# Kernel optimization log

Hardware: AMD Instinct MI355X
Metric: run time of the kernel (lower is better)

Reference implementation:

```python
import jax, jax.numpy as jnp
import numpy as np

LINK_LEN = 3
LN_EPS = 1e-5


def _layer_norm(x, w, b):
    mu = jnp.mean(x, axis=-1, keepdims=True)
    var = jnp.var(x, axis=-1, keepdims=True)
    return (x - mu) * jax.lax.rsqrt(var + LN_EPS) * w + b


def setup_inputs() -> dict:
    key = jax.random.key(0)
    ks = jax.random.split(key, 7)
    B, LAG, N, DIN, E, H = 16, 12, 5000, 32, 64, 64
    HH = H // 2
    return {
        "x": jax.random.normal(ks[0], (B, N, DIN), jnp.float32),
        "x_window": jax.random.normal(ks[1], (B, LAG, N, DIN // 2), jnp.float32),
        "node_embeddings": jax.random.normal(ks[2], (N, E), jnp.float32),
        "weights_pool": jax.random.normal(ks[3], (E, LINK_LEN, DIN, HH), jnp.float32) * 0.1,
        "weights_window": jax.random.normal(ks[4], (E, DIN // 2, HH), jnp.float32) * 0.1,
        "bias_pool": jax.random.normal(ks[5], (E, H), jnp.float32) * 0.1,
        "T": jax.random.normal(ks[6], (LAG,), jnp.float32),
        "ln1_w": jnp.ones((HH,), jnp.float32),
        "ln1_b": jnp.zeros((HH,), jnp.float32),
        "ln2_w": jnp.ones((HH,), jnp.float32),
        "ln2_b": jnp.zeros((HH,), jnp.float32),
    }


def reference(x, x_window, node_embeddings, weights_pool, weights_window,
              bias_pool, T, ln1_w, ln1_b, ln2_w, ln2_b):
    N = node_embeddings.shape[0]
    # adaptive adjacency: softmax(relu(E E^T)) over rows' neighbors (dim=1)
    supports = jax.nn.softmax(jax.nn.relu(node_embeddings @ node_embeddings.T), axis=1)
    support_set = [jnp.eye(N, dtype=x.dtype), supports]
    for k in range(2, LINK_LEN):
        support_set.append(supports @ support_set[k - 1])
    S = jnp.stack(support_set, axis=0)                      # [k, N, N]
    # per-node dynamic weights / bias from embeddings
    weights = jnp.einsum('nd,dkio->nkio', node_embeddings, weights_pool)  # [N,k,DIN,HH]
    bias = node_embeddings @ bias_pool                                     # [N,H]
    # graph conv path
    x_g = jnp.einsum('knm,bmc->bnkc', S, x)                 # [B,N,k,DIN]
    x_gconv = jnp.einsum('bnki,nkio->bno', x_g, weights)    # [B,N,HH]
    # temporal window path
    ww = jnp.einsum('nd,dio->nio', node_embeddings, weights_window)        # [N,DIN/2,HH]
    x_w = jnp.einsum('btni,nio->bnot', x_window, ww)        # [B,N,HH,LAG]
    x_wconv = x_w @ T                                       # [B,N,HH]
    out = jnp.concatenate([_layer_norm(x_gconv, ln1_w, ln1_b),
                           _layer_norm(x_wconv, ln2_w, ln2_b)], axis=-1) + bias
    return out
```

## Files before the change

kernel.cpp:

```cpp
#include <hip/hip_runtime.h>
#include <hip/hip_bf16.h>

#define NN   5000
#define EDIM 64
#define DINC 32
#define BB   16
#define LAGN 12
#define BC   512
#define KPAD 5120

typedef __attribute__((ext_vector_type(8))) short short8;
typedef __attribute__((ext_vector_type(4))) float float4v;

static __device__ __forceinline__ ushort f2bf(float x) {
  __hip_bfloat16 h = __float2bfloat16(x);
  return *reinterpret_cast<ushort*>(&h);
}
static __device__ __forceinline__ float bf2f(ushort u) {
  unsigned int x = ((unsigned int)u) << 16;
  return __uint_as_float(x);
}
static __device__ __forceinline__ short8 cvt8(const float* p) {
  const float4 v0 = *(const float4*)p, v1 = *(const float4*)(p + 4);
  short8 r;
  r[0] = (short)f2bf(v0.x); r[1] = (short)f2bf(v0.y);
  r[2] = (short)f2bf(v0.z); r[3] = (short)f2bf(v0.w);
  r[4] = (short)f2bf(v1.x); r[5] = (short)f2bf(v1.y);
  r[6] = (short)f2bf(v1.z); r[7] = (short)f2bf(v1.w);
  return r;
}

static __device__ __forceinline__ void gll16(const ushort* g, ushort* l) {
  __builtin_amdgcn_global_load_lds(
      (const __attribute__((address_space(1))) void*)g,
      (__attribute__((address_space(3))) void*)l, 16, 0, 0);
}


__global__ __launch_bounds__(256) void prep_kernel(const float* __restrict__ x,
                                                   const float* __restrict__ wpool,
                                                   const float* __restrict__ wwin,
                                                   const float* __restrict__ emb,
                                                   ushort* __restrict__ XbT,
                                                   float* __restrict__ wpP,
                                                   float* __restrict__ wwP,
                                                   ushort* __restrict__ eH,
                                                   ushort* __restrict__ eL) {
  const int b = blockIdx.x, tid = threadIdx.x;
  if (b < 10240) {
    const int j = b / 20, m = (b - j * 20) * 256 + tid;
    const int bb = j >> 5, c = j & 31;
    ushort v = 0;
    if (m < NN) v = f2bf(x[((size_t)bb * NN + m) * DINC + c]);
    XbT[(size_t)j * KPAD + m] = v;
  } else if (b < 11008) {
    const int t = (b - 10240) * 256 + tid;
    const int d = t / 3072, r = t - d * 3072;
    const int kk = r >> 10, r2 = r & 1023, i = r2 >> 5, o = r2 & 31;
    wpP[(size_t)d * 3072 + o * 96 + kk * 32 + i] = wpool[t];
  } else if (b < 11136) {
    const int t = (b - 11008) * 256 + tid;
    const int d = t >> 9, r = t & 511, i = r >> 5, o = r & 31;
    wwP[(size_t)d * 512 + o * 16 + i] = wwin[t];
  } else {
    const int t = (b - 11136) * 256 + tid;
    const int row = t >> 6;
    float v = 0.f;
    if (row < NN) v = emb[t];
    const ushort h = f2bf(v);
    eH[t] = h;
    eL[t] = f2bf(v - bf2f(h));
  }
}

__global__ __launch_bounds__(256) void fused_A_softmax_kernel(const ushort* __restrict__ eH,
                                                              const ushort* __restrict__ eL,
                                                              ushort* __restrict__ P,
                                                              ushort* __restrict__ scr) {
  __shared__ __align__(16) ushort Ls[32768];
  const int tid = threadIdx.x;
  const int w = tid >> 6, l = tid & 63;
  const int fm = l & 15, kq = l >> 4;
  const int rg = blockIdx.x >> 2, ch = blockIdx.x & 3;
  const int row0 = rg * 32;
  const int cbase = ch * 1280;
  __shared__ float redL[4][32];
  __shared__ float diagL[32];

  const int rstg = tid >> 3;
  const int slot = tid & 7;
  ushort* lH = Ls + tid * 8;
  ushort* lL = Ls + 8192 + tid * 8;

  auto stage = [&](int buf, int t) {
    const int c0 = cbase + t * 128;
#pragma unroll
    for (int q = 0; q < 4; ++q) {
      const int r = q * 32 + rstg;
      const int cg = slot ^ (r & 7);
      gll16(eH + (size_t)(c0 + r) * 64 + cg * 8, lH + buf * 16384 + q * 2048);
    }
#pragma unroll
    for (int q = 0; q < 4; ++q) {
      const int r = q * 32 + rstg;
      const int cg = slot ^ (r & 7);
      gll16(eL + (size_t)(c0 + r) * 64 + cg * 8, lL + buf * 16384 + q * 2048);
    }
  };

  short8 aH[2][2], aL[2][2];
#pragma unroll
  for (int mf = 0; mf < 2; ++mf)
#pragma unroll
    for (int s = 0; s < 2; ++s) {
      const size_t o = (size_t)(row0 + mf * 16 + fm) * 64 + (s * 4 + kq) * 8;
      aH[mf][s] = *(const short8*)(eH + o);
      aL[mf][s] = *(const short8*)(eL + o);
    }

  stage(0, 0);

#pragma unroll
  for (int mf = 0; mf < 2; ++mf) {
    float p = 0.f;
#pragma unroll
    for (int s = 0; s < 2; ++s)
#pragma unroll
      for (int j = 0; j < 8; ++j) {
        const float v = bf2f((ushort)aH[mf][s][j]) + bf2f((ushort)aL[mf][s][j]);
        p = fmaf(v, v, p);
      }
    p += __shfl_xor(p, 16);
    p += __shfl_xor(p, 32);
    if (w == 0 && kq == 0) diagL[mf * 16 + fm] = p;
  }
  __syncthreads();
  float shift[2][4];
#pragma unroll
  for (int mf = 0; mf < 2; ++mf)
#pragma unroll
    for (int r = 0; r < 4; ++r) shift[mf][r] = diagL[mf * 16 + kq * 4 + r];

  float rs[2][4] = {};
  ushort* prow[2][4];
#pragma unroll
  for (int mf = 0; mf < 2; ++mf)
#pragma unroll
    for (int r = 0; r < 4; ++r) {
      const int gm = row0 + mf * 16 + kq * 4 + r;
      prow[mf][r] = (gm < NN) ? (P + (size_t)gm * 10000 + (gm & 1) * 16) : scr;
    }

  auto compute = [&](int buf, int t) {
    const ushort* H = Ls + buf * 16384;
    const ushort* L = H + 8192;
    const int c0 = cbase + t * 128;
    float4v acc[2][2] = {};
#pragma unroll
    for (int s = 0; s < 2; ++s) {
      short8 bh[2], bl[2];
#pragma unroll
      for (int nf = 0; nf < 2; ++nf) {
        const int row = w * 32 + nf * 16 + fm;
        const int sl = (s * 4 + kq) ^ (fm & 7);
        bh[nf] = *(const short8*)(H + row * 64 + sl * 8);
        bl[nf] = *(const short8*)(L + row * 64 + sl * 8);
      }
#pragma unroll
      for (int mf = 0; mf < 2; ++mf)
#pragma unroll
        for (int nf = 0; nf < 2; ++nf) {
          acc[mf][nf] = __builtin_amdgcn_mfma_f32_16x16x32_bf16(aL[mf][s], bh[nf], acc[mf][nf], 0, 0, 0);
          acc[mf][nf] = __builtin_amdgcn_mfma_f32_16x16x32_bf16(aH[mf][s], bl[nf], acc[mf][nf], 0, 0, 0);
          acc[mf][nf] = __builtin_amdgcn_mfma_f32_16x16x32_bf16(aH[mf][s], bh[nf], acc[mf][nf], 0, 0, 0);
        }
    }
#pragma unroll
    for (int nf = 0; nf < 2; ++nf) {
      const int col = c0 + w * 32 + nf * 16 + fm;
      const bool ok = col < NN;
#pragma unroll
      for (int mf = 0; mf < 2; ++mf)
#pragma unroll
        for (int r = 0; r < 4; ++r) {
          const float v = fmaxf(acc[mf][nf][r], 0.f);
          const float e = ok ? __expf(v - shift[mf][r]) : 0.f;
          rs[mf][r] += e;
          prow[mf][r][col] = f2bf(e);
        }
    }
  };

  int cur = 0;
  for (int t = 0; t < 9; ++t) {
    stage(cur ^ 1, t + 1);
    compute(cur, t);
    __syncthreads();
    cur ^= 1;
  }
  compute(cur, 9);

#pragma unroll
  for (int mf = 0; mf < 2; ++mf)
#pragma unroll
    for (int r = 0; r < 4; ++r) {
      float v = rs[mf][r];
#pragma unroll
      for (int msk = 1; msk < 16; msk <<= 1) v += __shfl_xor(v, msk);
      rs[mf][r] = v;
    }
  __syncthreads();
  if (fm == 0) {
#pragma unroll
    for (int mf = 0; mf < 2; ++mf)
#pragma unroll
      for (int r = 0; r < 4; ++r) redL[w][mf * 16 + kq * 4 + r] = rs[mf][r];
  }
  __syncthreads();
  if (w == 0 && fm == 0) {
#pragma unroll
    for (int mf = 0; mf < 2; ++mf)
#pragma unroll
      for (int r = 0; r < 4; ++r) {
        const int mm = mf * 16 + kq * 4 + r;
        const int gm = row0 + mm;
        if (gm < NN) {
          const float tot = redL[0][mm] + redL[1][mm] + redL[2][mm] + redL[3][mm];
          *(float*)(P + (size_t)gm * 10000 + 9472 + 2 * ch) = tot;
        }
      }
  }
}

__global__ __launch_bounds__(256) void mfma_gemm_kernel(const ushort* __restrict__ Pm,
                                                        const ushort* __restrict__ Bt,
                                                        ushort* __restrict__ Pp) {
  __shared__ __align__(16) ushort Ls[32768];
  const int tid = threadIdx.x;
  const int w = tid >> 6, l = tid & 63;
  const int fm = l & 15, kq = l >> 4;
  const int wm = w >> 1, wn = w & 1;
  const int id = blockIdx.x;
  const int yb = id >> 5;
  const int xb = (id >> 3) & 3;
  const int zb = id & 7;
  const int row0 = yb * 128, col0 = xb * 128;
  const int kbase = zb * 640;
  const int rstg = tid >> 3;
  const int slot = tid & 7;
  const ushort* gAq[4];
  const ushort* gBq[4];
#pragma unroll
  for (int q = 0; q < 4; ++q) {
    const int r = q * 32 + rstg;
    const int cg = slot ^ (r & 7);
    const int arow = row0 + r;
    gAq[q] = Pm + (size_t)arow * 10000 + (arow & 1) * 16 + kbase + cg * 8;
    gBq[q] = Bt + (size_t)(col0 + r) * KPAD + kbase + cg * 8;
  }
  ushort* lA = Ls + tid * 8;
  ushort* lB = Ls + 8192 + tid * 8;
  float4v acc[4][4] = {};

  auto stage = [&](int buf) {
#pragma unroll
    for (int q = 0; q < 4; ++q) gll16(gAq[q], lA + buf * 16384 + q * 2048);
#pragma unroll
    for (int q = 0; q < 4; ++q) gll16(gBq[q], lB + buf * 16384 + q * 2048);
#pragma unroll
    for (int q = 0; q < 4; ++q) { gAq[q] += 64; gBq[q] += 64; }
  };
  auto compute = [&](int buf) {
    const ushort* As = Ls + buf * 16384;
    const ushort* Bs = As + 8192;
#pragma unroll
    for (int s = 0; s < 2; ++s) {
      short8 a[4], b[4];
#pragma unroll
      for (int mt = 0; mt < 4; ++mt) {
        const int row = wm * 64 + mt * 16 + fm;
        const int sl = (s * 4 + kq) ^ (fm & 7);
        a[mt] = *(const short8*)(As + row * 64 + sl * 8);
      }
#pragma unroll
      for (int nt = 0; nt < 4; ++nt) {
        const int row = wn * 64 + nt * 16 + fm;
        const int sl = (s * 4 + kq) ^ (fm & 7);
        b[nt] = *(const short8*)(Bs + row * 64 + sl * 8);
      }
#pragma unroll
      for (int mt = 0; mt < 4; ++mt)
#pragma unroll
        for (int nt = 0; nt < 4; ++nt)
          acc[mt][nt] = __builtin_amdgcn_mfma_f32_16x16x32_bf16(a[mt], b[nt], acc[mt][nt], 0, 0, 0);
    }
  };

  stage(0);
  __syncthreads();
  int cur = 0;
  for (int kt = 0; kt < 9; ++kt) {
    stage(cur ^ 1);
    compute(cur);
    __syncthreads();
    cur ^= 1;
  }
  compute(cur);

  const int cb = col0 + wn * 64 + fm;
  const int zoff = 5160 + zb * 512;
#pragma unroll
  for (int mt = 0; mt < 4; ++mt)
#pragma unroll
    for (int r = 0; r < 4; ++r) {
      const int gm = row0 + wm * 64 + mt * 16 + kq * 4 + r;
      if (gm < NN) {
        ushort* prow = Pp + (size_t)gm * 10000 + zoff + cb;
#pragma unroll
        for (int nt = 0; nt < 4; ++nt) prow[nt * 16] = f2bf(acc[mt][nt][r]);
      }
    }
}

__global__ __launch_bounds__(256) void reduce_kernel(const ushort* __restrict__ Pp,
                                                     float* __restrict__ Yf,
                                                     ushort* __restrict__ Yt,
                                                     int writeT) {
  const int m0 = blockIdx.y * 64, n0 = blockIdx.x * 64;
  __shared__ __align__(16) ushort Lt[64][80];
  const int tid = threadIdx.x;
  const int mi = tid >> 4, nl4 = (tid & 15) << 2;
#pragma unroll
  for (int s = 0; s < 4; ++s) {
    const int m = m0 + mi + s * 16;
    float4 sum = make_float4(0.f, 0.f, 0.f, 0.f);
    if (m < NN) {
      const ushort* pr = Pp + (size_t)m * 10000 + 5160 + n0 + nl4;
#pragma unroll
      for (int z = 0; z < 8; ++z) {
        ushort4 u = *(const ushort4*)(pr + z * 512);
        sum.x += bf2f(u.x); sum.y += bf2f(u.y);
        sum.z += bf2f(u.z); sum.w += bf2f(u.w);
      }
      const float4 s4 = *(const float4*)(Pp + (size_t)m * 10000 + 9472);
      const float sc = 1.f / (s4.x + s4.y + s4.z + s4.w);
      sum.x *= sc; sum.y *= sc; sum.z *= sc; sum.w *= sc;
      *(float4*)(Yf + (size_t)m * BC + n0 + nl4) = sum;
    }
    if (writeT) {
      const int ml = mi + s * 16;
      Lt[nl4 + 0][ml] = f2bf(sum.x);
      Lt[nl4 + 1][ml] = f2bf(sum.y);
      Lt[nl4 + 2][ml] = f2bf(sum.z);
      Lt[nl4 + 3][ml] = f2bf(sum.w);
    }
  }
  if (writeT) {
    __syncthreads();
#pragma unroll
    for (int i = 0; i < 2; ++i) {
      const int g = tid + i * 256;
      const int nl = g >> 3, gi = g & 7;
      *(uint4*)(Yt + (size_t)(n0 + nl) * KPAD + m0 + gi * 8) =
          *(const uint4*)(&Lt[nl][gi * 8]);
    }
  }
}

__global__ __launch_bounds__(256) void emb_gemm_bf16_kernel(const float* __restrict__ Ae,
                                                            const float* __restrict__ Bp,
                                                            ushort* __restrict__ C,
                                                            int Nc) {
  __shared__ float Aet[EDIM][33];
  __shared__ __align__(16) float Bs[EDIM][64];
  const int row0 = blockIdx.y * 32, col0 = blockIdx.x * 64;
  const int tid = threadIdx.x;
  for (int i = tid; i < 512; i += 256) {
    const int r = i >> 4, d4 = (i & 15) << 2;
    const int gm = row0 + r;
    float4 v = make_float4(0.f, 0.f, 0.f, 0.f);
    if (gm < NN) v = *(const float4*)(Ae + (size_t)gm * EDIM + d4);
    Aet[d4 + 0][r] = v.x; Aet[d4 + 1][r] = v.y; Aet[d4 + 2][r] = v.z; Aet[d4 + 3][r] = v.w;
  }
  for (int i = tid; i < 1024; i += 256) {
    const int br = i >> 4, bc = (i & 15) << 2;
    *(float4*)&Bs[br][bc] = *(const float4*)(Bp + (size_t)br * Nc + col0 + bc);
  }
  __syncthreads();
  const int ty = tid >> 4, tx = tid & 15;
  float acc[2][4] = {};
#pragma unroll 8
  for (int d = 0; d < EDIM; ++d) {
    const float a0 = Aet[d][ty * 2], a1 = Aet[d][ty * 2 + 1];
    const float4 b4 = *(const float4*)&Bs[d][tx << 2];
    acc[0][0] = fmaf(a0, b4.x, acc[0][0]); acc[0][1] = fmaf(a0, b4.y, acc[0][1]);
    acc[0][2] = fmaf(a0, b4.z, acc[0][2]); acc[0][3] = fmaf(a0, b4.w, acc[0][3]);
    acc[1][0] = fmaf(a1, b4.x, acc[1][0]); acc[1][1] = fmaf(a1, b4.y, acc[1][1]);
    acc[1][2] = fmaf(a1, b4.z, acc[1][2]); acc[1][3] = fmaf(a1, b4.w, acc[1][3]);
  }
#pragma unroll
  for (int r = 0; r < 2; ++r) {
    const int gm = row0 + ty * 2 + r;
    if (gm >= NN) continue;
    ushort4 o4;
    o4.x = f2bf(acc[r][0]); o4.y = f2bf(acc[r][1]);
    o4.z = f2bf(acc[r][2]); o4.w = f2bf(acc[r][3]);
    *(ushort4*)(C + (size_t)gm * Nc + col0 + (tx << 2)) = o4;
  }
}

__global__ __launch_bounds__(256) void emb_gemm_kernel(const float* __restrict__ Ae,
                                                       const float* __restrict__ Bw,
                                                       float* __restrict__ C,
                                                       int M, int Nc) {
  __shared__ float Aet[EDIM][33];
  __shared__ __align__(16) float Bs[EDIM][64];
  const int row0 = blockIdx.y * 32, col0 = blockIdx.x * 64;
  const int tid = threadIdx.x;
  for (int i = tid; i < 512; i += 256) {
    const int r = i >> 4, d4 = (i & 15) << 2;
    const int gm = row0 + r;
    float4 v = make_float4(0.f, 0.f, 0.f, 0.f);
    if (gm < M) v = *(const float4*)(Ae + (size_t)gm * EDIM + d4);
    Aet[d4 + 0][r] = v.x; Aet[d4 + 1][r] = v.y; Aet[d4 + 2][r] = v.z; Aet[d4 + 3][r] = v.w;
  }
  for (int i = tid; i < 1024; i += 256) {
    const int br = i >> 4, bc = (i & 15) << 2;
    if (bc < Nc) *(float4*)&Bs[br][bc] = *(const float4*)(Bw + (size_t)br * Nc + bc);
  }
  __syncthreads();
  const int ty = tid >> 4, tx = tid & 15;
  float acc[2][4] = {};
#pragma unroll 8
  for (int d = 0; d < EDIM; ++d) {
    const float a0 = Aet[d][ty * 2], a1 = Aet[d][ty * 2 + 1];
    const float4 b4 = *(const float4*)&Bs[d][tx << 2];
    acc[0][0] = fmaf(a0, b4.x, acc[0][0]); acc[0][1] = fmaf(a0, b4.y, acc[0][1]);
    acc[0][2] = fmaf(a0, b4.z, acc[0][2]); acc[0][3] = fmaf(a0, b4.w, acc[0][3]);
    acc[1][0] = fmaf(a1, b4.x, acc[1][0]); acc[1][1] = fmaf(a1, b4.y, acc[1][1]);
    acc[1][2] = fmaf(a1, b4.z, acc[1][2]); acc[1][3] = fmaf(a1, b4.w, acc[1][3]);
  }
#pragma unroll
  for (int r = 0; r < 2; ++r) {
    const int gm = row0 + ty * 2 + r;
    if (gm >= M) continue;
    float4 o;
    o.x = acc[r][0]; o.y = acc[r][1]; o.z = acc[r][2]; o.w = acc[r][3];
    *(float4*)(C + (size_t)gm * Nc + col0 + (tx << 2)) = o;
  }
}

__global__ __launch_bounds__(256) void window_combine_kernel(const float* __restrict__ xw,
                                                             const float* __restrict__ T,
                                                             float* __restrict__ out) {
  const int idx = blockIdx.x * 256 + threadIdx.x;
  if (idx >= BB * NN * 16) return;
  const int b = idx / (NN * 16);
  const int rem = idx - b * (NN * 16);
  float acc = 0.f;
#pragma unroll
  for (int t = 0; t < LAGN; ++t)
    acc = fmaf(T[t], xw[(size_t)(b * LAGN + t) * (NN * 16) + rem], acc);
  out[idx] = acc;
}

__global__ __launch_bounds__(256) void fuse_mfma_kernel(const float* __restrict__ x,
                                                        const float* __restrict__ Y1f,
                                                        const float* __restrict__ Y2f,
                                                        const ushort* __restrict__ Wt,
                                                        const ushort* __restrict__ wwt,
                                                        const float* __restrict__ biasN,
                                                        const float* __restrict__ xwc,
                                                        const float* __restrict__ ln1w,
                                                        const float* __restrict__ ln1b,
                                                        const float* __restrict__ ln2w,
                                                        const float* __restrict__ ln2b,
                                                        float* __restrict__ out) {
  const int tid = threadIdx.x;
  const int n = blockIdx.x * 4 + (tid >> 6);
  const int l = tid & 63, fm = l & 15, kq = l >> 4;
  const short8 ax = cvt8(x + ((size_t)fm * NN + n) * DINC + kq * 8);
  const short8 a1 = cvt8(Y1f + (size_t)n * BC + fm * 32 + kq * 8);
  const short8 a2 = cvt8(Y2f + (size_t)n * BC + fm * 32 + kq * 8);
  short8 aw = {};
  if (kq < 2) aw = cvt8(xwc + ((size_t)fm * NN + n) * 16 + kq * 8);
  const ushort* wn = Wt + (size_t)n * 3072;
  const ushort* wwn = wwt + (size_t)n * 512;
  float4v accG[2] = {}, accW[2] = {};
#pragma unroll
  for (int t = 0; t < 2; ++t) {
    const int ob = (t * 16 + fm) * 96 + kq * 8;
    const short8 b0 = *(const short8*)(wn + ob);
    const short8 b1 = *(const short8*)(wn + ob + 32);
    const short8 b2 = *(const short8*)(wn + ob + 64);
    accG[t] = __builtin_amdgcn_mfma_f32_16x16x32_bf16(ax, b0, accG[t], 0, 0, 0);
    accG[t] = __builtin_amdgcn_mfma_f32_16x16x32_bf16(a1, b1, accG[t], 0, 0, 0);
    accG[t] = __builtin_amdgcn_mfma_f32_16x16x32_bf16(a2, b2, accG[t], 0, 0, 0);
    short8 bw = {};
    if (kq < 2) bw = *(const short8*)(wwn + (t * 16 + fm) * 16 + kq * 8);
    accW[t] = __builtin_amdgcn_mfma_f32_16x16x32_bf16(aw, bw, accW[t], 0, 0, 0);
  }
  const float w1a = ln1w[fm], w1b = ln1w[16 + fm];
  const float c1a = ln1b[fm], c1b = ln1b[16 + fm];
  const float w2a = ln2w[fm], w2b = ln2w[16 + fm];
  const float c2a = ln2b[fm], c2b = ln2b[16 + fm];
  const float* bn = biasN + (size_t)n * 64;
  const float bga = bn[fm], bgb = bn[16 + fm];
  const float bwa = bn[32 + fm], bwb = bn[48 + fm];
#pragma unroll
  for (int r = 0; r < 4; ++r) {
    const int b = kq * 4 + r;
    const float g0 = accG[0][r], g1 = accG[1][r];
    float s1 = g0 + g1, s2 = g0 * g0 + g1 * g1;
#pragma unroll
    for (int m = 1; m < 16; m <<= 1) { s1 += __shfl_xor(s1, m); s2 += __shfl_xor(s2, m); }
    const float mu = s1 * 0.03125f;
    const float rs = rsqrtf(s2 * 0.03125f - mu * mu + 1e-5f);
    const float h0 = accW[0][r], h1 = accW[1][r];
    float t1 = h0 + h1, t2 = h0 * h0 + h1 * h1;
#pragma unroll
    for (int m = 1; m < 16; m <<= 1) { t1 += __shfl_xor(t1, m); t2 += __shfl_xor(t2, m); }
    const float mu2 = t1 * 0.03125f;
    const float rs2 = rsqrtf(t2 * 0.03125f - mu2 * mu2 + 1e-5f);
    float* op = out + ((size_t)b * NN + n) * 64;
    op[fm]      = (g0 - mu) * rs * w1a + c1a + bga;
    op[16 + fm] = (g1 - mu) * rs * w1b + c1b + bgb;
    op[32 + fm] = (h0 - mu2) * rs2 * w2a + c2a + bwa;
    op[48 + fm] = (h1 - mu2) * rs2 * w2b + c2b + bwb;
  }
}

extern "C" void kernel_launch(void* const* d_in, const int* in_sizes, int n_in,
                              void* d_out, int out_size, void* d_ws, size_t ws_size,
                              hipStream_t stream) {
  const float* x     = (const float*)d_in[0];
  const float* xwin  = (const float*)d_in[1];
  const float* emb   = (const float*)d_in[2];
  const float* wpool = (const float*)d_in[3];
  const float* wwin  = (const float*)d_in[4];
  const float* bpool = (const float*)d_in[5];
  const float* T     = (const float*)d_in[6];
  const float* ln1w  = (const float*)d_in[7];
  const float* ln1b  = (const float*)d_in[8];
  const float* ln2w  = (const float*)d_in[9];
  const float* ln2b  = (const float*)d_in[10];
  float* out = (float*)d_out;
  float* ws = (float*)d_ws;

  ushort* P    = (ushort*)ws;
  ushort* XbT  = (ushort*)(ws + 25000000);
  ushort* Y1t  = (ushort*)(ws + 26310720);
  float*  Y1f  = ws + 27621440;
  float*  Y2f  = ws + 25000000;
  ushort* embH = (ushort*)(ws + 27621440);
  ushort* embL = (ushort*)(ws + 27785280);
  ushort* ascr = (ushort*)(ws + 27949120);
  ushort* Wt    = (ushort*)ws;
  ushort* wwt   = (ushort*)(ws + 15360000);
  float*  biasN = ws + 17920000;
  float*  xwc   = ws + 18240000;
  float*  wpP   = ws + 30181440;
  float*  wwP   = ws + 30378048;

  prep_kernel<<<12416, 256, 0, stream>>>(x, wpool, wwin, emb, XbT, wpP, wwP, embH, embL);
  fused_A_softmax_kernel<<<628, 256, 0, stream>>>(embH, embL, P, ascr);
  mfma_gemm_kernel<<<1280, 256, 0, stream>>>(P, XbT, P);
  reduce_kernel<<<dim3(8, 80), 256, 0, stream>>>(P, Y1f, Y1t, 1);
  mfma_gemm_kernel<<<1280, 256, 0, stream>>>(P, Y1t, P);
  reduce_kernel<<<dim3(8, 80), 256, 0, stream>>>(P, Y2f, (ushort*)nullptr, 0);
  emb_gemm_bf16_kernel<<<dim3(48, 157), 256, 0, stream>>>(emb, wpP, Wt, 3072);
  emb_gemm_bf16_kernel<<<dim3(8, 157), 256, 0, stream>>>(emb, wwP, wwt, 512);
  emb_gemm_kernel<<<dim3(1, 157), 256, 0, stream>>>(emb, bpool, biasN, NN, 64);
  window_combine_kernel<<<(BB * NN * 16 + 255) / 256, 256, 0, stream>>>(xwin, T, xwc);
  fuse_mfma_kernel<<<1250, 256, 0, stream>>>(x, Y1f, Y2f, Wt, wwt, biasN, xwc,
                                             ln1w, ln1b, ln2w, ln2b, out);
}
```

Measured before the change: 359.3 us.

## Merge per-node weight generation GEMMs into one split-bf16 MFMA kernel

Replaces the two fp32 FMA embedding-weight GEMMs (pool weights and window weights) with a single MFMA kernel. It uses a hi/lo bf16 split (three MFMAs per tile) to keep near-fp32 accuracy, and the prep kernel now emits transposed hi/lo bf16 weight copies. The aim is to cut the scalar-FMA cost of producing the 5000x3584 per-node weights and to save one launch. In exchange the kernel does three times the MFMA work and writes its output as scattered 2-byte stores.

After: 335.7 us. -6.6%, faster.

```diff
diff --git a/kernel.cpp b/kernel.cpp
--- a/kernel.cpp
+++ b/kernel.cpp
@@ -42,8 +42,8 @@
                                                    const float* __restrict__ wwin,
                                                    const float* __restrict__ emb,
                                                    ushort* __restrict__ XbT,
-                                                   float* __restrict__ wpP,
-                                                   float* __restrict__ wwP,
+                                                   ushort* __restrict__ wtH,
+                                                   ushort* __restrict__ wtL,
                                                    ushort* __restrict__ eH,
                                                    ushort* __restrict__ eL) {
   const int b = blockIdx.x, tid = threadIdx.x;
@@ -55,13 +55,20 @@
     XbT[(size_t)j * KPAD + m] = v;
   } else if (b < 11008) {
     const int t = (b - 10240) * 256 + tid;
-    const int d = t / 3072, r = t - d * 3072;
-    const int kk = r >> 10, r2 = r & 1023, i = r2 >> 5, o = r2 & 31;
-    wpP[(size_t)d * 3072 + o * 96 + kk * 32 + i] = wpool[t];
+    const int col = t >> 6, d = t & 63;
+    const int o = col / 96, r2 = col - o * 96, kk = r2 >> 5, i = r2 & 31;
+    const float v = wpool[(size_t)d * 3072 + kk * 1024 + i * 32 + o];
+    const ushort h = f2bf(v);
+    wtH[t] = h;
+    wtL[t] = f2bf(v - bf2f(h));
   } else if (b < 11136) {
     const int t = (b - 11008) * 256 + tid;
-    const int d = t >> 9, r = t & 511, i = r >> 5, o = r & 31;
-    wwP[(size_t)d * 512 + o * 16 + i] = wwin[t];
+    const int col = t >> 6, d = t & 63;
+    const int o = col >> 4, i = col & 15;
+    const float v = wwin[(size_t)d * 512 + i * 32 + o];
+    const ushort h = f2bf(v);
+    wtH[196608 + t] = h;
+    wtL[196608 + t] = f2bf(v - bf2f(h));
   } else {
     const int t = (b - 11136) * 256 + tid;
     const int row = t >> 6;
@@ -367,45 +374,74 @@
   }
 }
 
-__global__ __launch_bounds__(256) void emb_gemm_bf16_kernel(const float* __restrict__ Ae,
-                                                            const float* __restrict__ Bp,
-                                                            ushort* __restrict__ C,
-                                                            int Nc) {
-  __shared__ float Aet[EDIM][33];
-  __shared__ __align__(16) float Bs[EDIM][64];
-  const int row0 = blockIdx.y * 32, col0 = blockIdx.x * 64;
+__global__ __launch_bounds__(256) void emb_wt_mfma_kernel(const float* __restrict__ emb,
+                                                          const ushort* __restrict__ wtH,
+                                                          const ushort* __restrict__ wtL,
+                                                          ushort* __restrict__ Wt,
+                                                          ushort* __restrict__ wwt) {
   const int tid = threadIdx.x;
-  for (int i = tid; i < 512; i += 256) {
-    const int r = i >> 4, d4 = (i & 15) << 2;
-    const int gm = row0 + r;
-    float4 v = make_float4(0.f, 0.f, 0.f, 0.f);
-    if (gm < NN) v = *(const float4*)(Ae + (size_t)gm * EDIM + d4);
-    Aet[d4 + 0][r] = v.x; Aet[d4 + 1][r] = v.y; Aet[d4 + 2][r] = v.z; Aet[d4 + 3][r] = v.w;
-  }
-  for (int i = tid; i < 1024; i += 256) {
-    const int br = i >> 4, bc = (i & 15) << 2;
-    *(float4*)&Bs[br][bc] = *(const float4*)(Bp + (size_t)br * Nc + col0 + bc);
-  }
-  __syncthreads();
-  const int ty = tid >> 4, tx = tid & 15;
-  float acc[2][4] = {};
-#pragma unroll 8
-  for (int d = 0; d < EDIM; ++d) {
-    const float a0 = Aet[d][ty * 2], a1 = Aet[d][ty * 2 + 1];
-    const float4 b4 = *(const float4*)&Bs[d][tx << 2];
-    acc[0][0] = fmaf(a0, b4.x, acc[0][0]); acc[0][1] = fmaf(a0, b4.y, acc[0][1]);
-    acc[0][2] = fmaf(a0, b4.z, acc[0][2]); acc[0][3] = fmaf(a0, b4.w, acc[0][3]);
-    acc[1][0] = fmaf(a1, b4.x, acc[1][0]); acc[1][1] = fmaf(a1, b4.y, acc[1][1]);
-    acc[1][2] = fmaf(a1, b4.z, acc[1][2]); acc[1][3] = fmaf(a1, b4.w, acc[1][3]);
-  }
-#pragma unroll
-  for (int r = 0; r < 2; ++r) {
-    const int gm = row0 + ty * 2 + r;
-    if (gm >= NN) continue;
-    ushort4 o4;
-    o4.x = f2bf(acc[r][0]); o4.y = f2bf(acc[r][1]);
-    o4.z = f2bf(acc[r][2]); o4.w = f2bf(acc[r][3]);
-    *(ushort4*)(C + (size_t)gm * Nc + col0 + (tx << 2)) = o4;
+  const int w = tid >> 6, l = tid & 63;
+  const int fm = l & 15, kq = l >> 4;
+  const int rg = blockIdx.x / 14, cc = blockIdx.x % 14;
+  const int row0 = rg * 32;
+  const int c0 = cc * 256 + w * 64;
+
+  short8 aH[2][2], aL[2][2];
+#pragma unroll
+  for (int mf = 0; mf < 2; ++mf) {
+    const int gr = row0 + mf * 16 + fm;
+#pragma unroll
+    for (int s = 0; s < 2; ++s) {
+      short8 h = {}, lo = {};
+      if (gr < NN) {
+        const float* p = emb + (size_t)gr * EDIM + (s * 4 + kq) * 8;
+        const float4 v0 = *(const float4*)p, v1 = *(const float4*)(p + 4);
+        const float vv[8] = {v0.x, v0.y, v0.z, v0.w, v1.x, v1.y, v1.z, v1.w};
+#pragma unroll
+        for (int j = 0; j < 8; ++j) {
+          const ushort hh = f2bf(vv[j]);
+          h[j] = (short)hh;
+          lo[j] = (short)f2bf(vv[j] - bf2f(hh));
+        }
+      }
+      aH[mf][s] = h;
+      aL[mf][s] = lo;
+    }
+  }
+
+  float4v acc[2][4] = {};
+#pragma unroll
+  for (int s = 0; s < 2; ++s) {
+    short8 bh[4], bl[4];
+#pragma unroll
+    for (int nf = 0; nf < 4; ++nf) {
+      const size_t o = (size_t)(c0 + nf * 16 + fm) * 64 + (s * 4 + kq) * 8;
+      bh[nf] = *(const short8*)(wtH + o);
+      bl[nf] = *(const short8*)(wtL + o);
+    }
+#pragma unroll
+    for (int mf = 0; mf < 2; ++mf)
+#pragma unroll
+      for (int nf = 0; nf < 4; ++nf) {
+        acc[mf][nf] = __builtin_amdgcn_mfma_f32_16x16x32_bf16(aL[mf][s], bh[nf], acc[mf][nf], 0, 0, 0);
+        acc[mf][nf] = __builtin_amdgcn_mfma_f32_16x16x32_bf16(aH[mf][s], bl[nf], acc[mf][nf], 0, 0, 0);
+        acc[mf][nf] = __builtin_amdgcn_mfma_f32_16x16x32_bf16(aH[mf][s], bh[nf], acc[mf][nf], 0, 0, 0);
+      }
+  }
+#pragma unroll
+  for (int nf = 0; nf < 4; ++nf) {
+    const int col = c0 + nf * 16 + fm;
+#pragma unroll
+    for (int mf = 0; mf < 2; ++mf)
+#pragma unroll
+      for (int r = 0; r < 4; ++r) {
+        const int gm = row0 + mf * 16 + kq * 4 + r;
+        if (gm < NN) {
+          const ushort v = f2bf(acc[mf][nf][r]);
+          if (col < 3072) Wt[(size_t)gm * 3072 + col] = v;
+          else            wwt[(size_t)gm * 512 + (col - 3072)] = v;
+        }
+      }
   }
 }
 
@@ -559,17 +595,16 @@
   ushort* wwt   = (ushort*)(ws + 15360000);
   float*  biasN = ws + 17920000;
   float*  xwc   = ws + 18240000;
-  float*  wpP   = ws + 30181440;
-  float*  wwP   = ws + 30378048;
-
-  prep_kernel<<<12416, 256, 0, stream>>>(x, wpool, wwin, emb, XbT, wpP, wwP, embH, embL);
+  ushort* wtH   = (ushort*)(ws + 30181440);
+  ushort* wtL   = (ushort*)(ws + 30296128);
+
+  prep_kernel<<<12416, 256, 0, stream>>>(x, wpool, wwin, emb, XbT, wtH, wtL, embH, embL);
   fused_A_softmax_kernel<<<628, 256, 0, stream>>>(embH, embL, P, ascr);
   mfma_gemm_kernel<<<1280, 256, 0, stream>>>(P, XbT, P);
   reduce_kernel<<<dim3(8, 80), 256, 0, stream>>>(P, Y1f, Y1t, 1);
   mfma_gemm_kernel<<<1280, 256, 0, stream>>>(P, Y1t, P);
   reduce_kernel<<<dim3(8, 80), 256, 0, stream>>>(P, Y2f, (ushort*)nullptr, 0);
-  emb_gemm_bf16_kernel<<<dim3(48, 157), 256, 0, stream>>>(emb, wpP, Wt, 3072);
-  emb_gemm_bf16_kernel<<<dim3(8, 157), 256, 0, stream>>>(emb, wwP, wwt, 512);
+  emb_wt_mfma_kernel<<<2198, 256, 0, stream>>>(emb, wtH, wtL, Wt, wwt);
   emb_gemm_kernel<<<dim3(1, 157), 256, 0, stream>>>(emb, bpool, biasN, NN, 64);
   window_combine_kernel<<<(BB * NN * 16 + 255) / 256, 256, 0, stream>>>(xwin, T, xwc);
   fuse_mfma_kernel<<<1250, 256, 0, stream>>>(x, Y1f, Y2f, Wt, wwt, biasN, xwc,
```
